# Kernel tuning notes

Measured on AMD Instinct MI355X. Metric: run time of the kernel, lower is better.

The kernel has to match this reference:

```python
import jax, jax.numpy as jnp
import numpy as np

N, K, M, C, OUT, S = 80000, 8, 1000, 128, 64, 2
EPS = 1e-5


def _bn(x, g, b, m, v):
    # eval-mode BatchNorm1d applied over the last (channel) axis
    return (x - m) * (g / jnp.sqrt(v + EPS)) + b


def setup_inputs() -> dict:
    key = jax.random.key(0)
    ks = jax.random.split(key, 40)
    it = iter(range(40))
    rn = lambda sh, s=1.0: jax.random.normal(ks[next(it)], sh, dtype=jnp.float32) * s
    ru = lambda sh: jax.random.uniform(ks[next(it)], sh, dtype=jnp.float32, minval=0.5, maxval=1.5)
    w = 0.05
    inp = {}
    inp["sp_fea"] = rn((M, C))
    inp["sp_xyz"] = rn((M, 3))
    inp["o_p_fea"] = rn((N, C))
    inp["p_xyz"] = rn((N, 3))
    # linear_q / linear_k / linear_v  (in_planes -> mid_planes)
    inp["Wq"] = rn((C, C), w); inp["bq"] = jnp.zeros((C,), jnp.float32)
    inp["Wk"] = rn((C, C), w); inp["bk"] = jnp.zeros((C,), jnp.float32)
    inp["Wv"] = rn((C, C), w); inp["bv"] = jnp.zeros((C,), jnp.float32)
    # linear_p: Linear(3,3) -> BN(3) -> ReLU -> Linear(3, mid)
    inp["Wp1"] = rn((3, 3), 0.5); inp["bp1"] = jnp.zeros((3,), jnp.float32)
    inp["gp"] = 1.0 + rn((3,), 0.1); inp["betap"] = rn((3,), 0.1)
    inp["mp"] = rn((3,), 0.1); inp["vp"] = ru((3,))
    inp["Wp2"] = rn((3, C), 0.3); inp["bp2"] = jnp.zeros((C,), jnp.float32)
    # linear_w: BN(mid) -> ReLU -> Linear(mid,out) -> BN(out) -> ReLU -> Linear(out,out)
    inp["g1"] = 1.0 + rn((C,), 0.1); inp["beta1"] = rn((C,), 0.1)
    inp["m1"] = rn((C,), 0.1); inp["v1"] = ru((C,))
    inp["W1"] = rn((C, OUT), w); inp["b1"] = jnp.zeros((OUT,), jnp.float32)
    inp["g2"] = 1.0 + rn((OUT,), 0.1); inp["beta2"] = rn((OUT,), 0.1)
    inp["m2"] = rn((OUT,), 0.1); inp["v2"] = ru((OUT,))
    inp["W2"] = rn((OUT, OUT), w); inp["b2"] = jnp.zeros((OUT,), jnp.float32)
    # index / offset inputs (ints)
    inp["c2p_idx_abs"] = jax.random.randint(ks[next(it)], (N, K), 0, M)
    inp["c2p_idx"] = jax.random.randint(ks[next(it)], (N, K), 0, M)
    inp["cluster_idx"] = jax.random.randint(ks[next(it)], (N,), 0, M)
    inp["offset"] = jnp.array([N], dtype=jnp.int32)
    inp["sp_offset"] = jnp.array([M], dtype=jnp.int32)
    return inp


def reference(sp_fea, sp_xyz, o_p_fea, p_xyz,
              Wq, bq, Wk, bk, Wv, bv,
              Wp1, bp1, gp, betap, mp, vp, Wp2, bp2,
              g1, beta1, m1, v1, W1, b1,
              g2, beta2, m2, v2, W2, b2,
              c2p_idx_abs, c2p_idx, cluster_idx, offset, sp_offset):
    q = o_p_fea @ Wq + bq                               # [N, C]
    k_sp = (sp_fea @ Wk + bk)[c2p_idx_abs]              # gather -> [N, K, C]
    v_sp = (sp_fea @ Wv + bv)[c2p_idx_abs]              # [N, K, C]
    p_e = sp_xyz[c2p_idx_abs]                           # [N, K, 3]
    # positional encoding MLP
    p_e = jax.nn.relu(_bn(p_e @ Wp1 + bp1, gp, betap, mp, vp)) @ Wp2 + bp2  # [N, K, C]
    # vector attention scores
    w = k_sp - q[:, None, :] + p_e                      # [N, K, C]
    w = jax.nn.relu(_bn(w, g1, beta1, m1, v1)) @ W1 + b1
    w = jax.nn.relu(_bn(w, g2, beta2, m2, v2)) @ W2 + b2  # [N, K, OUT]
    w = jax.nn.softmax(w, axis=1)                        # softmax over the K neighbors
    # shared-plane weighted sum
    bi = ((v_sp + p_e).reshape(N, K, S, C // S) * w[:, :, None, :]).reshape(N, K, C)
    bi = bi.sum(axis=2)                                  # [N, K]
    return jax.nn.softmax(bi, axis=1)                    # association matrix [N, K]
```

## Files before the change

kernel.cpp:

```cpp
#include <hip/hip_runtime.h>
#include <stdint.h>

#define EPS 1e-5f
#define LOG2E 1.4426950408889634f

#define NPTS 80000
#define CDIM 128
#define ODIM 64
#define KNBR 8
#define MSUP 1000

#define KP2H_OFF 0
#define UT_OFF   (256*1024)
#define WQF_OFF  (512*1024)
#define W1F_OFF  (544*1024)
#define W2F_OFF  (560*1024)
#define C1_OFF   (568*1024)
#define WSTAGE_BYTES (16*1024 + 8*1024 + 256)

typedef float f32x4 __attribute__((ext_vector_type(4)));
typedef _Float16 f16x8 __attribute__((ext_vector_type(8)));
typedef _Float16 f16x4 __attribute__((ext_vector_type(4)));
typedef _Float16 f16x2 __attribute__((ext_vector_type(2)));

union FragU { f16x8 v; unsigned u[4]; uint4 q; };

__device__ inline unsigned pk_f16(float lo, float hi) {
#if __has_builtin(__builtin_amdgcn_cvt_pkrtz)
  return __builtin_bit_cast(unsigned, __builtin_amdgcn_cvt_pkrtz(lo, hi));
#else
  f16x2 h;
  h[0] = (_Float16)lo;
  h[1] = (_Float16)hi;
  return __builtin_bit_cast(unsigned, h);
#endif
}

__device__ inline float exp2_fast(float x) {
#if __has_builtin(__builtin_amdgcn_exp2f)
  return __builtin_amdgcn_exp2f(x);
#else
  return exp2f(x);
#endif
}

__device__ inline float row16_sum(float v) {
  float acc = v;
#if __has_builtin(__builtin_amdgcn_update_dpp)
  #define DPP_ADD(CTRL) {                                                     \
    int t_ = __builtin_amdgcn_update_dpp(0, __builtin_bit_cast(int, acc),     \
                                         (CTRL), 0xf, 0xf, true);             \
    acc += __builtin_bit_cast(float, t_); }
  DPP_ADD(0x128)
  DPP_ADD(0x124)
  DPP_ADD(0x122)
  DPP_ADD(0x121)
  #undef DPP_ADD
#else
  acc += __shfl_xor(acc, 8);
  acc += __shfl_xor(acc, 4);
  acc += __shfl_xor(acc, 2);
  acc += __shfl_xor(acc, 1);
#endif
  return acc;
}

__global__ __launch_bounds__(256)
void k_prep(const float* __restrict__ sp_fea, const float* __restrict__ sp_xyz,
            const float* __restrict__ Wk, const float* __restrict__ bk,
            const float* __restrict__ Wv, const float* __restrict__ bv,
            const float* __restrict__ Wp1, const float* __restrict__ bp1,
            const float* __restrict__ gp, const float* __restrict__ betap,
            const float* __restrict__ mp, const float* __restrict__ vp,
            const float* __restrict__ Wp2, const float* __restrict__ bp2,
            const float* __restrict__ g1, const float* __restrict__ beta1,
            const float* __restrict__ m1, const float* __restrict__ v1,
            const float* __restrict__ bq,
            const float* __restrict__ Wq, const float* __restrict__ W1,
            const float* __restrict__ W2,
            const float* __restrict__ g2, const float* __restrict__ v2,
            const float* __restrict__ b1, const float* __restrict__ m2,
            const float* __restrict__ beta2, char* __restrict__ ws)
{
  if (blockIdx.x < 1000) {
    unsigned short* kp2h = (unsigned short*)(ws + KP2H_OFF);
    float* uT = (float*)(ws + UT_OFF);
    const int m = blockIdx.x;
    const int t = threadIdx.x;
    const int c = t & 127, half = t >> 7;
    __shared__ float fea[128];
    __shared__ float pk[128], pv[128];
    if (t < 128) fea[t] = sp_fea[m * 128 + t];
    __syncthreads();
    float kv = 0.f, vv = 0.f;
    const float* wkc = Wk + half * 64 * 128 + c;
    const float* wvc = Wv + half * 64 * 128 + c;
    const float* feah = fea + half * 64;
    #pragma unroll 8
    for (int d = 0; d < 64; ++d) {
      const float f = feah[d];
      kv = fmaf(f, wkc[d * 128], kv);
      vv = fmaf(f, wvc[d * 128], vv);
    }
    if (half) { pk[c] = kv; pv[c] = vv; }
    __syncthreads();
    if (!half) {
      kv += pk[c] + bk[c];
      vv += pv[c] + bv[c];
      const float x0 = sp_xyz[m*3+0], x1 = sp_xyz[m*3+1], x2 = sp_xyz[m*3+2];
      float pe = bp2[c];
      #pragma unroll
      for (int ii = 0; ii < 3; ++ii) {
        float s = bp1[ii] + x0*Wp1[0*3+ii] + x1*Wp1[1*3+ii] + x2*Wp1[2*3+ii];
        s = (s - mp[ii]) * (gp[ii] * rsqrtf(vp[ii] + EPS)) + betap[ii];
        s = fmaxf(s, 0.0f);
        pe += s * Wp2[ii*128 + c];
      }
      const float s1c = g1[c] * rsqrtf(v1[c] + EPS);
      const float kpv = (kv + pe - m1[c] - bq[c]) * s1c + beta1[c];
      kp2h[m*128 + c] = (unsigned short)(pk_f16(kpv, kpv) & 0xFFFFu);
      pv[c] = vv + pe;
    }
    __syncthreads();
    if (t < 64) {
      const int j = (t >> 2) + (t & 3) * 16;
      uT[m*64 + t] = (pv[j] + pv[j + 64]) * LOG2E;
    }
  } else {
    const int tid = (blockIdx.x - 1000) * 256 + threadIdx.x;
    if (tid < 2048) {
      const int e = tid, f = e >> 6, l = e & 63;
      const int kt = f >> 3, mt = f & 7;
      const int c = mt*16 + (l & 15);
      const int d0 = kt*32 + (l >> 4)*8;
      const float sc = g1[c] * rsqrtf(v1[c] + EPS);
      uint4 u;
      u.x = pk_f16(Wq[(d0+0)*128 + c]*sc, Wq[(d0+1)*128 + c]*sc);
      u.y = pk_f16(Wq[(d0+2)*128 + c]*sc, Wq[(d0+3)*128 + c]*sc);
      u.z = pk_f16(Wq[(d0+4)*128 + c]*sc, Wq[(d0+5)*128 + c]*sc);
      u.w = pk_f16(Wq[(d0+6)*128 + c]*sc, Wq[(d0+7)*128 + c]*sc);
      *(uint4*)(ws + WQF_OFF + e*16) = u;
    } else if (tid < 3072) {
      const int e = tid - 2048, f = e >> 6, l = e & 63;
      const int kt = f >> 2, jt = f & 3;
      const int j = jt*16 + (l & 15);
      const int c0 = kt*32 + (l >> 4)*8;
      const float sc = g2[j] * rsqrtf(v2[j] + EPS);
      uint4 u;
      u.x = pk_f16(W1[(c0+0)*64 + j]*sc, W1[(c0+1)*64 + j]*sc);
      u.y = pk_f16(W1[(c0+2)*64 + j]*sc, W1[(c0+3)*64 + j]*sc);
      u.z = pk_f16(W1[(c0+4)*64 + j]*sc, W1[(c0+5)*64 + j]*sc);
      u.w = pk_f16(W1[(c0+6)*64 + j]*sc, W1[(c0+7)*64 + j]*sc);
      *(uint4*)(ws + W1F_OFF + e*16) = u;
    } else if (tid < 3584) {
      const int e = tid - 3072, f = e >> 6, l = e & 63;
      const int kt2 = f >> 2, nt = f & 3;
      const int jp = nt*16 + (l & 15);
      const int j0 = kt2*32 + (l >> 4)*8;
      uint4 u;
      u.x = pk_f16(W2[(j0+0)*64 + jp]*LOG2E, W2[(j0+1)*64 + jp]*LOG2E);
      u.y = pk_f16(W2[(j0+2)*64 + jp]*LOG2E, W2[(j0+3)*64 + jp]*LOG2E);
      u.z = pk_f16(W2[(j0+4)*64 + jp]*LOG2E, W2[(j0+5)*64 + jp]*LOG2E);
      u.w = pk_f16(W2[(j0+6)*64 + jp]*LOG2E, W2[(j0+7)*64 + jp]*LOG2E);
      *(uint4*)(ws + W2F_OFF + e*16) = u;
    } else if (tid < 3648) {
      const int j = tid - 3584;
      const float sc = g2[j] * rsqrtf(v2[j] + EPS);
      ((float*)(ws + C1_OFF))[j] = (b1[j] - m2[j]) * sc + beta2[j];
    }
  }
}

#define H2_PITCH 144
#define H2_SIZE  (16*144)
#define W1L_OFF  0
#define W2L_OFF  (16*1024)
#define C1L_OFF  (24*1024)
#define H2_BASE  24832
#define QL_OFF   (H2_BASE + 4*H2_SIZE)
#define QL_PITCH 272
#define LDS_TOTAL (QL_OFF + 32*QL_PITCH)

__global__ __launch_bounds__(256, 3)
void k_main(const int* __restrict__ idx, const float* __restrict__ b2,
            const float* __restrict__ o_p_fea,
            const char* __restrict__ ws, float* __restrict__ out)
{
  const unsigned short* kp2h = (const unsigned short*)(ws + KP2H_OFF);
  const float* uT = (const float*)(ws + UT_OFF);

  __shared__ __align__(16) char lds[LDS_TOTAL];
  const int t = threadIdx.x;
  const int wave = t >> 6, l = t & 63;
  const int quad = l >> 4, row = l & 15;
  char* h2_w = lds + H2_BASE + wave * H2_SIZE;

  const int slot = blockIdx.x * 4 + wave;
  const int gid0 = slot * 4;
  const int nloc = row >> 3;

  {
    const uint4* src = (const uint4*)(ws + W1F_OFF);
    uint4* dst = (uint4*)lds;
    #pragma unroll
    for (int i = 0; i < 7; ++i) {
      const int e = t + i * 256;
      if (e < WSTAGE_BYTES / 16) dst[e] = src[e];
    }
  }

  {
    const int tile = wave >> 1;
    const int mt0 = (wave & 1) * 4;
    const int nq = blockIdx.x * 32 + tile * 16 + row;
    const float* feab = o_p_fea + (size_t)nq * 128;
    f32x4 qa[4];
    #pragma unroll
    for (int mt = 0; mt < 4; ++mt) qa[mt] = (f32x4){0.f, 0.f, 0.f, 0.f};
    #pragma unroll
    for (int kt = 0; kt < 4; ++kt) {
      f32x4 fa = *(const f32x4*)(feab + kt*32 + quad*8);
      f32x4 fb = *(const f32x4*)(feab + kt*32 + quad*8 + 4);
      FragU bu;
      bu.u[0] = pk_f16(fa[0], fa[1]);
      bu.u[1] = pk_f16(fa[2], fa[3]);
      bu.u[2] = pk_f16(fb[0], fb[1]);
      bu.u[3] = pk_f16(fb[2], fb[3]);
      #pragma unroll
      for (int mt = 0; mt < 4; ++mt) {
        FragU wf;
        wf.q = *(const uint4*)(ws + WQF_OFF + (((kt*8 + mt0 + mt)*64 + l) * 16));
        qa[mt] = __builtin_amdgcn_mfma_f32_16x16x32_f16(wf.v, bu.v, qa[mt], 0, 0, 0);
      }
    }
    char* lq = lds + QL_OFF + (tile*16 + row) * QL_PITCH;
    #pragma unroll
    for (int mt = 0; mt < 4; ++mt) {
      uint2 pp;
      pp.x = pk_f16(qa[mt][0], qa[mt][1]);
      pp.y = pk_f16(qa[mt][2], qa[mt][3]);
      *(uint2*)(lq + (mt0 + mt)*32 + quad*8) = pp;
    }
  }

  int mr4[4];
  #pragma unroll
  for (int g = 0; g < 4; ++g) mr4[g] = idx[(gid0 + g)*16 + row];

  __syncthreads();

  f32x4 c1r[4];
  #pragma unroll
  for (int jt = 0; jt < 4; ++jt)
    c1r[jt] = *(const f32x4*)(lds + C1L_OFF + (jt*16 + quad*4)*4);
  float b2r[4];
  #pragma unroll
  for (int nt = 0; nt < 4; ++nt) b2r[nt] = b2[row + nt*16] * LOG2E;

  int msc[4];
  #pragma unroll
  for (int rg = 0; rg < 4; ++rg) msc[rg] = idx[gid0*16 + quad*4 + rg];
  uint4 kfc[4];
  {
    const uint4* kr = (const uint4*)(kp2h + (size_t)mr4[0] * 128);
    #pragma unroll
    for (int kt = 0; kt < 4; ++kt) kfc[kt] = kr[kt*4 + quad];
  }
  uint4 qpc[4];
  {
    const char* lqr = lds + QL_OFF + (wave*8 + nloc) * QL_PITCH;
    #pragma unroll
    for (int kt = 0; kt < 4; ++kt)
      qpc[kt] = *(const uint4*)(lqr + (kt*4 + quad)*16);
  }

  #pragma unroll 1
  for (int g = 0; g < 4; ++g) {
    const int gid = gid0 + g;
    int msn[4];
    uint4 kfn[4];
    if (g < 3) {
      #pragma unroll
      for (int rg = 0; rg < 4; ++rg) msn[rg] = idx[(gid+1)*16 + quad*4 + rg];
      const uint4* kr = (const uint4*)(kp2h + (size_t)mr4[g+1] * 128);
      #pragma unroll
      for (int kt = 0; kt < 4; ++kt) kfn[kt] = kr[kt*4 + quad];
    }

    f32x4 a1[4];
    #pragma unroll
    for (int jt = 0; jt < 4; ++jt) a1[jt] = c1r[jt];
    #pragma unroll
    for (int kt = 0; kt < 4; ++kt) {
      const f16x8 kv = __builtin_bit_cast(f16x8, kfc[kt]);
      const f16x8 qv = __builtin_bit_cast(f16x8, qpc[kt]);
      f16x8 z = {};
      f16x8 x = __builtin_elementwise_max((f16x8)(kv - qv), z);
      FragU xf;
      xf.v = x;
      #pragma unroll
      for (int jt = 0; jt < 4; ++jt) {
        const f16x8 wf = *(const f16x8*)(lds + W1L_OFF + (kt*4+jt)*1024 + l*16);
        a1[jt] = __builtin_amdgcn_mfma_f32_16x16x32_f16(wf, xf.v, a1[jt], 0, 0, 0);
      }
    }

    #pragma unroll
    for (int jt = 0; jt < 4; ++jt) {
      uint2 pp;
      pp.x = pk_f16(a1[jt][0], a1[jt][1]);
      pp.y = pk_f16(a1[jt][2], a1[jt][3]);
      f16x4 h = __builtin_bit_cast(f16x4, pp);
      f16x4 z4 = {};
      h = __builtin_elementwise_max(h, z4);
      pp = __builtin_bit_cast(uint2, h);
      *(uint2*)(h2_w + row*H2_PITCH + (jt*16 + quad*4)*2) = pp;
    }

    uint4 qpn[4];
    if (g < 3) {
      const char* lqr = lds + QL_OFF + (wave*8 + (g+1)*2 + nloc) * QL_PITCH;
      #pragma unroll
      for (int kt = 0; kt < 4; ++kt)
        qpn[kt] = *(const uint4*)(lqr + (kt*4 + quad)*16);
    }

    f32x4 u4[4];
    #pragma unroll
    for (int rg = 0; rg < 4; ++rg)
      u4[rg] = *(const f32x4*)(uT + (size_t)msc[rg] * 64 + row * 4);

    f32x4 a2[4];
    #pragma unroll
    for (int nt = 0; nt < 4; ++nt) a2[nt] = (f32x4){0.f, 0.f, 0.f, 0.f};
    #pragma unroll
    for (int kt2 = 0; kt2 < 2; ++kt2) {
      const f16x8 af = *(const f16x8*)(h2_w + row*H2_PITCH + kt2*64 + quad*16);
      #pragma unroll
      for (int nt = 0; nt < 4; ++nt) {
        const f16x8 wf = *(const f16x8*)(lds + W2L_OFF + (kt2*4+nt)*1024 + l*16);
        a2[nt] = __builtin_amdgcn_mfma_f32_16x16x32_f16(af, wf, a2[nt], 0, 0, 0);
      }
    }
    float bi0 = 0.f, bi1 = 0.f, bi2 = 0.f, bi3 = 0.f;
    #pragma unroll
    for (int nt = 0; nt < 4; ++nt) {
      const float e0 = exp2_fast(a2[nt][0] + b2r[nt]);
      const float e1 = exp2_fast(a2[nt][1] + b2r[nt]);
      const float e2 = exp2_fast(a2[nt][2] + b2r[nt]);
      const float e3 = exp2_fast(a2[nt][3] + b2r[nt]);
      float s = e0 + e1 + e2 + e3;
      s += __shfl_xor(s, 16);
      const float rs = __builtin_amdgcn_rcpf(s);
      bi0 = fmaf(e0 * rs, u4[0][nt], bi0);
      bi1 = fmaf(e1 * rs, u4[1][nt], bi1);
      bi2 = fmaf(e2 * rs, u4[2][nt], bi2);
      bi3 = fmaf(e3 * rs, u4[3][nt], bi3);
    }
    float bi[4];
    bi[0] = row16_sum(bi0);
    bi[1] = row16_sum(bi1);
    bi[2] = row16_sum(bi2);
    bi[3] = row16_sum(bi3);
    const float eb0 = exp2_fast(bi[0]), eb1 = exp2_fast(bi[1]);
    const float eb2 = exp2_fast(bi[2]), eb3 = exp2_fast(bi[3]);
    float sb = eb0 + eb1 + eb2 + eb3;
    sb += __shfl_xor(sb, 16);
    const float rsb = __builtin_amdgcn_rcpf(sb);
    if (row < 4) {
      const float vsel = row == 0 ? eb0 : row == 1 ? eb1 : row == 2 ? eb2 : eb3;
      out[gid*16 + quad*4 + row] = vsel * rsb;
    }
    if (g < 3) {
      #pragma unroll
      for (int rg = 0; rg < 4; ++rg) msc[rg] = msn[rg];
      #pragma unroll
      for (int kt = 0; kt < 4; ++kt) { kfc[kt] = kfn[kt]; qpc[kt] = qpn[kt]; }
    }
  }
}

extern "C" void kernel_launch(void* const* d_in, const int* in_sizes, int n_in,
                              void* d_out, int out_size, void* d_ws, size_t ws_size,
                              hipStream_t stream)
{
  const float* sp_fea  = (const float*)d_in[0];
  const float* sp_xyz  = (const float*)d_in[1];
  const float* o_p_fea = (const float*)d_in[2];
  const float* Wq    = (const float*)d_in[4];
  const float* bq    = (const float*)d_in[5];
  const float* Wk    = (const float*)d_in[6];
  const float* bk    = (const float*)d_in[7];
  const float* Wv    = (const float*)d_in[8];
  const float* bv    = (const float*)d_in[9];
  const float* Wp1   = (const float*)d_in[10];
  const float* bp1   = (const float*)d_in[11];
  const float* gp    = (const float*)d_in[12];
  const float* betap = (const float*)d_in[13];
  const float* mp    = (const float*)d_in[14];
  const float* vp    = (const float*)d_in[15];
  const float* Wp2   = (const float*)d_in[16];
  const float* bp2   = (const float*)d_in[17];
  const float* g1    = (const float*)d_in[18];
  const float* beta1 = (const float*)d_in[19];
  const float* m1    = (const float*)d_in[20];
  const float* v1    = (const float*)d_in[21];
  const float* W1    = (const float*)d_in[22];
  const float* b1    = (const float*)d_in[23];
  const float* g2    = (const float*)d_in[24];
  const float* beta2 = (const float*)d_in[25];
  const float* m2    = (const float*)d_in[26];
  const float* v2    = (const float*)d_in[27];
  const float* W2    = (const float*)d_in[28];
  const float* b2    = (const float*)d_in[29];
  const int* c2p_idx_abs = (const int*)d_in[30];

  char* ws = (char*)d_ws;
  float* out = (float*)d_out;

  hipLaunchKernelGGL(k_prep, dim3(1015), dim3(256), 0, stream,
                     sp_fea, sp_xyz, Wk, bk, Wv, bv, Wp1, bp1, gp, betap, mp, vp,
                     Wp2, bp2, g1, beta1, m1, v1, bq,
                     Wq, W1, W2, g2, v2, b1, m2, beta2, ws);
  hipLaunchKernelGGL(k_main, dim3(2500), dim3(256), 0, stream,
                     c2p_idx_abs, b2, o_p_fea, ws, out);
}
```

Baseline: 196.7 us.

## Software-pipeline GEMM1 and GEMM2 across groups with double-buffered H2 LDS tiles

Restructures the per-wave group loop so the second GEMM plus softmax for group g runs before the first GEMM for group g+1. The hidden activations are double-buffered in LDS so the two stages do not conflict. The aim is to overlap MFMA chains and LDS traffic from independent groups and hide latency. In exchange the H2 LDS region doubles, which may reduce occupancy at three blocks per CU, and the prologue and epilogue add code size.

```diff
diff --git a/kernel.cpp b/kernel.cpp
--- a/kernel.cpp
+++ b/kernel.cpp
@@ -177,7 +177,7 @@
 #define W2L_OFF  (16*1024)
 #define C1L_OFF  (24*1024)
 #define H2_BASE  24832
-#define QL_OFF   (H2_BASE + 4*H2_SIZE)
+#define QL_OFF   (H2_BASE + 8*H2_SIZE)
 #define QL_PITCH 272
 #define LDS_TOTAL (QL_OFF + 32*QL_PITCH)
 
@@ -193,7 +193,7 @@
   const int t = threadIdx.x;
   const int wave = t >> 6, l = t & 63;
   const int quad = l >> 4, row = l & 15;
-  char* h2_w = lds + H2_BASE + wave * H2_SIZE;
+  char* h2base = lds + H2_BASE + wave * (2 * H2_SIZE);
 
   const int slot = blockIdx.x * 4 + wave;
   const int gid0 = slot * 4;
@@ -257,43 +257,25 @@
   #pragma unroll
   for (int nt = 0; nt < 4; ++nt) b2r[nt] = b2[row + nt*16] * LOG2E;
 
-  int msc[4];
-  #pragma unroll
-  for (int rg = 0; rg < 4; ++rg) msc[rg] = idx[gid0*16 + quad*4 + rg];
-  uint4 kfc[4];
-  {
-    const uint4* kr = (const uint4*)(kp2h + (size_t)mr4[0] * 128);
-    #pragma unroll
-    for (int kt = 0; kt < 4; ++kt) kfc[kt] = kr[kt*4 + quad];
-  }
-  uint4 qpc[4];
-  {
-    const char* lqr = lds + QL_OFF + (wave*8 + nloc) * QL_PITCH;
+  auto qload = [&](int g, uint4* qp) {
+    const char* lqr = lds + QL_OFF + (wave*8 + g*2 + nloc) * QL_PITCH;
     #pragma unroll
     for (int kt = 0; kt < 4; ++kt)
-      qpc[kt] = *(const uint4*)(lqr + (kt*4 + quad)*16);
-  }
-
-  #pragma unroll 1
-  for (int g = 0; g < 4; ++g) {
-    const int gid = gid0 + g;
-    int msn[4];
-    uint4 kfn[4];
-    if (g < 3) {
-      #pragma unroll
-      for (int rg = 0; rg < 4; ++rg) msn[rg] = idx[(gid+1)*16 + quad*4 + rg];
-      const uint4* kr = (const uint4*)(kp2h + (size_t)mr4[g+1] * 128);
-      #pragma unroll
-      for (int kt = 0; kt < 4; ++kt) kfn[kt] = kr[kt*4 + quad];
-    }
-
+      qp[kt] = *(const uint4*)(lqr + (kt*4 + quad)*16);
+  };
+  auto kload = [&](int g, uint4* kf) {
+    const uint4* kr = (const uint4*)(kp2h + (size_t)mr4[g] * 128);
+    #pragma unroll
+    for (int kt = 0; kt < 4; ++kt) kf[kt] = kr[kt*4 + quad];
+  };
+  auto run_gemm1 = [&](const uint4* kf, const uint4* qp, char* h2dst) {
     f32x4 a1[4];
     #pragma unroll
     for (int jt = 0; jt < 4; ++jt) a1[jt] = c1r[jt];
     #pragma unroll
     for (int kt = 0; kt < 4; ++kt) {
-      const f16x8 kv = __builtin_bit_cast(f16x8, kfc[kt]);
-      const f16x8 qv = __builtin_bit_cast(f16x8, qpc[kt]);
+      const f16x8 kv = __builtin_bit_cast(f16x8, kf[kt]);
+      const f16x8 qv = __builtin_bit_cast(f16x8, qp[kt]);
       f16x8 z = {};
       f16x8 x = __builtin_elementwise_max((f16x8)(kv - qv), z);
       FragU xf;
@@ -304,7 +286,6 @@
         a1[jt] = __builtin_amdgcn_mfma_f32_16x16x32_f16(wf, xf.v, a1[jt], 0, 0, 0);
       }
     }
-
     #pragma unroll
     for (int jt = 0; jt < 4; ++jt) {
       uint2 pp;
@@ -314,28 +295,16 @@
       f16x4 z4 = {};
       h = __builtin_elementwise_max(h, z4);
       pp = __builtin_bit_cast(uint2, h);
-      *(uint2*)(h2_w + row*H2_PITCH + (jt*16 + quad*4)*2) = pp;
-    }
-
-    uint4 qpn[4];
-    if (g < 3) {
-      const char* lqr = lds + QL_OFF + (wave*8 + (g+1)*2 + nloc) * QL_PITCH;
-      #pragma unroll
-      for (int kt = 0; kt < 4; ++kt)
-        qpn[kt] = *(const uint4*)(lqr + (kt*4 + quad)*16);
-    }
-
-    f32x4 u4[4];
-    #pragma unroll
-    for (int rg = 0; rg < 4; ++rg)
-      u4[rg] = *(const f32x4*)(uT + (size_t)msc[rg] * 64 + row * 4);
-
+      *(uint2*)(h2dst + row*H2_PITCH + (jt*16 + quad*4)*2) = pp;
+    }
+  };
+  auto run_gemm2 = [&](const char* h2src, const f32x4* u4, int gid) {
     f32x4 a2[4];
     #pragma unroll
     for (int nt = 0; nt < 4; ++nt) a2[nt] = (f32x4){0.f, 0.f, 0.f, 0.f};
     #pragma unroll
     for (int kt2 = 0; kt2 < 2; ++kt2) {
-      const f16x8 af = *(const f16x8*)(h2_w + row*H2_PITCH + kt2*64 + quad*16);
+      const f16x8 af = *(const f16x8*)(h2src + row*H2_PITCH + kt2*64 + quad*16);
       #pragma unroll
       for (int nt = 0; nt < 4; ++nt) {
         const f16x8 wf = *(const f16x8*)(lds + W2L_OFF + (kt2*4+nt)*1024 + l*16);
@@ -371,12 +340,48 @@
       const float vsel = row == 0 ? eb0 : row == 1 ? eb1 : row == 2 ? eb2 : eb3;
       out[gid*16 + quad*4 + row] = vsel * rsb;
     }
-    if (g < 3) {
+  };
+
+  int msc[4];
+  #pragma unroll
+  for (int rg = 0; rg < 4; ++rg) msc[rg] = idx[gid0*16 + quad*4 + rg];
+  uint4 kfn[4], qpn[4];
+  kload(0, kfn);
+  qload(0, qpn);
+  run_gemm1(kfn, qpn, h2base);
+  int msn[4];
+  #pragma unroll
+  for (int rg = 0; rg < 4; ++rg) msn[rg] = idx[(gid0+1)*16 + quad*4 + rg];
+  kload(1, kfn);
+  qload(1, qpn);
+
+  #pragma unroll 1
+  for (int g = 0; g < 3; ++g) {
+    f32x4 u4[4];
+    #pragma unroll
+    for (int rg = 0; rg < 4; ++rg)
+      u4[rg] = *(const f32x4*)(uT + (size_t)msc[rg] * 64 + row * 4);
+
+    run_gemm2(h2base + (g & 1) * H2_SIZE, u4, gid0 + g);
+
+    run_gemm1(kfn, qpn, h2base + ((g + 1) & 1) * H2_SIZE);
+
+    #pragma unroll
+    for (int rg = 0; rg < 4; ++rg) msc[rg] = msn[rg];
+    if (g < 2) {
       #pragma unroll
-      for (int rg = 0; rg < 4; ++rg) msc[rg] = msn[rg];
-      #pragma unroll
-      for (int kt = 0; kt < 4; ++kt) { kfc[kt] = kfn[kt]; qpc[kt] = qpn[kt]; }
-    }
+      for (int rg = 0; rg < 4; ++rg) msn[rg] = idx[(gid0+g+2)*16 + quad*4 + rg];
+      kload(g + 2, kfn);
+      qload(g + 2, qpn);
+    }
+  }
+
+  {
+    f32x4 u4[4];
+    #pragma unroll
+    for (int rg = 0; rg < 4; ++rg)
+      u4[rg] = *(const f32x4*)(uT + (size_t)msc[rg] * 64 + row * 4);
+    run_gemm2(h2base + H2_SIZE, u4, gid0 + 3);
   }
 }
 
```

Measured after the change: 194.4 us. Within noise of the previous version (-1.1%).
